# Optimization experiments

Hardware: AMD Instinct MI355X
Metric: run time of the kernel (lower is better)

Reference implementation:

```python
import jax, jax.numpy as jnp
import numpy as np

B, N, D, E = 2, 50000, 64, 800000


def setup_inputs() -> dict:
    key = jax.random.key(0)
    k = jax.random.split(key, 6)
    return {
        "prev_embeddings": jax.random.normal(k[0], (B, N, D), dtype=jnp.float32),
        "edges_ij": jax.random.randint(k[1], (E, 2), 0, N, dtype=jnp.int64 if jax.config.jax_enable_x64 else jnp.int32),
        "node_features_embeddings": jax.random.normal(k[2], (B, N, D), dtype=jnp.float32),
        "edge_features_embeddings": jax.random.normal(k[3], (B, N, D), dtype=jnp.float32),
        "edge_status": jax.random.uniform(k[4], (E,), dtype=jnp.float32),
        "W": jax.random.normal(k[5], (D, D), dtype=jnp.float32) / np.sqrt(D).astype(np.float32),
    }


def reference(prev_embeddings, edges_ij, node_features_embeddings, edge_features_embeddings, edge_status, W):
    # prev_embeddings: (B, N, D); edges_ij: (E, 2); edge_status: (E,) in [0,1]; W: (D, D) theta2 weight (no bias)
    u = edges_ij[:, 0]
    v = edges_ij[:, 1]
    g = edge_status.astype(prev_embeddings.dtype).reshape(1, -1, 1)  # broadcast (1,E,1) over batch
    h_u = prev_embeddings[:, u, :] * g  # gather source endpoint, gate
    h_v = prev_embeddings[:, v, :] * g  # gather dest endpoint, gate
    # scatter-add gated messages in both directions: nbr[b, v] += h_u, nbr[b, u] += h_v
    nbr = jnp.zeros_like(prev_embeddings).at[:, v, :].add(h_u).at[:, u, :].add(h_v)
    x2 = jnp.einsum('bnd,ed->bne', nbr, W)  # Linear(D,D,bias=False): nbr @ W.T
    return jax.nn.leaky_relu(node_features_embeddings + x2 + edge_features_embeddings)
```

## Files before the change

kernel.cpp:

```cpp
#include <hip/hip_runtime.h>

constexpr int B = 2;
constexpr int N = 50000;
constexpr int D = 64;
constexpr int E = 800000;
constexpr int CAP = 96;
constexpr int XG = 8;
constexpr int NPG = N / XG;
constexpr int ECHUNKS = E / 256;

constexpr int ROWS_PER_WAVE = 25;
constexpr int PGROUPS = 125;
constexpr int TOTAL_GROUPS = ECHUNKS + PGROUPS;

__device__ __forceinline__ unsigned f2bf(float f) {
    unsigned u = __float_as_uint(f);
    return (u + 0x7FFFu + ((u >> 16) & 1u)) >> 16;
}
__device__ __forceinline__ float bfhi2f(unsigned bits) {
    return __uint_as_float(bits & 0xFFFF0000u);
}
__device__ __forceinline__ float bflo2f(unsigned bits) {
    return __uint_as_float(bits << 16);
}

__global__ __launch_bounds__(256) void build_pgemm_fused(
    const int2* __restrict__ edges, const float* __restrict__ status,
    int* __restrict__ counts, unsigned* __restrict__ slots,
    const float* __restrict__ prev, const float* __restrict__ W,
    unsigned* __restrict__ P32)
{
    int grp = blockIdx.x >> 3;
    int sub8 = blockIdx.x & 7;
    int t = threadIdx.x;

    int nm = grp / 26;
    int pos = grp % 26;

    if (pos < 25) {
        int chunk = nm * 25 + pos;
        int e = chunk * 256 + t;
        int2 uv = edges[e];
        unsigned gb = f2bf(status[e]) << 16;
        if (uv.x / NPG == sub8) {
            int p = atomicAdd(&counts[uv.x], 1);
            if (p < CAP) slots[(size_t)uv.x * CAP + p] = gb | (unsigned)uv.y;
        }
        if (uv.y / NPG == sub8) {
            int p = atomicAdd(&counts[uv.y], 1);
            if (p < CAP) slots[(size_t)uv.y * CAP + p] = gb | (unsigned)uv.x;
        }
    } else {
        int pb = nm * 8 + sub8;
        int wave = t >> 6, lane = t & 63;

        const float4* W4 = (const float4*)W;
        float4 w[16];
#pragma unroll
        for (int q = 0; q < 16; ++q) w[q] = W4[lane * 16 + q];

        int row0 = pb * (4 * ROWS_PER_WAVE) + wave * ROWS_PER_WAVE;
        for (int r = 0; r < ROWS_PER_WAVE; ++r) {
            int row = __builtin_amdgcn_readfirstlane(row0 + r);
            const float* pr = prev + (size_t)row * D;

            float acc = 0.f;
#pragma unroll
            for (int d = 0; d < D; ++d) {
                const float4& wq = w[d >> 2];
                float wd = (d & 3) == 0 ? wq.x : (d & 3) == 1 ? wq.y
                         : (d & 3) == 2 ? wq.z : wq.w;
                acc += pr[d] * wd;
            }

            float partner = __shfl_xor(acc, 1, 64);
            if ((lane & 1) == 0) {
                P32[(size_t)row * 32 + (lane >> 1)] = f2bf(acc) | (f2bf(partner) << 16);
            }
        }
    }
}

__global__ __launch_bounds__(256) void gather_final(
    const uint4* __restrict__ P4,
    const int* __restrict__ counts,
    const unsigned* __restrict__ slots,
    const float* __restrict__ node,
    const float* __restrict__ edgef,
    float* __restrict__ out)
{
    __shared__ float xs[4][2][D];

    int t = threadIdx.x;
    int wave = t >> 6, lane = t & 63;
    int n = blockIdx.x * 4 + wave;
    int j = lane & 7;
    int sub = lane >> 3;

    int cnt = min(counts[n], CAP);
    size_t sbase = (size_t)n * CAP;

    float a0[8], a1[8];
#pragma unroll
    for (int i = 0; i < 8; ++i) { a0[i] = 0.f; a1[i] = 0.f; }

    for (int k = sub; k < cnt; k += 8) {
        unsigned ent = slots[sbase + k];
        float g = bfhi2f(ent);
        unsigned nb = ent & 0xFFFFu;
        uint4 r0 = P4[(size_t)nb * 8 + j];
        uint4 r1 = P4[((size_t)N + nb) * 8 + j];
        a0[0] += g * bflo2f(r0.x); a0[1] += g * bfhi2f(r0.x);
        a0[2] += g * bflo2f(r0.y); a0[3] += g * bfhi2f(r0.y);
        a0[4] += g * bflo2f(r0.z); a0[5] += g * bfhi2f(r0.z);
        a0[6] += g * bflo2f(r0.w); a0[7] += g * bfhi2f(r0.w);
        a1[0] += g * bflo2f(r1.x); a1[1] += g * bfhi2f(r1.x);
        a1[2] += g * bflo2f(r1.y); a1[3] += g * bfhi2f(r1.y);
        a1[4] += g * bflo2f(r1.z); a1[5] += g * bfhi2f(r1.z);
        a1[6] += g * bflo2f(r1.w); a1[7] += g * bfhi2f(r1.w);
    }

#pragma unroll
    for (int m = 8; m <= 32; m <<= 1) {
#pragma unroll
        for (int i = 0; i < 8; ++i) {
            a0[i] += __shfl_xor(a0[i], m, 64);
            a1[i] += __shfl_xor(a1[i], m, 64);
        }
    }

    if (sub == 0) {
        *(float4*)&xs[wave][0][j * 8]     = make_float4(a0[0], a0[1], a0[2], a0[3]);
        *(float4*)&xs[wave][0][j * 8 + 4] = make_float4(a0[4], a0[5], a0[6], a0[7]);
        *(float4*)&xs[wave][1][j * 8]     = make_float4(a1[0], a1[1], a1[2], a1[3]);
        *(float4*)&xs[wave][1][j * 8 + 4] = make_float4(a1[4], a1[5], a1[6], a1[7]);
    }
    float s0 = xs[wave][0][lane];
    float s1 = xs[wave][1][lane];

    size_t b0 = (size_t)n * D + lane;
    size_t b1 = (size_t)N * D + b0;
    float y0 = node[b0] + s0 + edgef[b0];
    float y1 = node[b1] + s1 + edgef[b1];
    out[b0] = (y0 >= 0.f) ? y0 : 0.01f * y0;
    out[b1] = (y1 >= 0.f) ? y1 : 0.01f * y1;
}

__device__ inline void atomic_add4(float* p, float4 val, float g) {
    atomicAdd(p + 0, val.x * g);
    atomicAdd(p + 1, val.y * g);
    atomicAdd(p + 2, val.z * g);
    atomicAdd(p + 3, val.w * g);
}

__global__ __launch_bounds__(256) void scatter_kernel(
    const float* __restrict__ prev,
    const int2* __restrict__ edges,
    const float* __restrict__ status,
    float* __restrict__ nbr)
{
    int idx = blockIdx.x * 256 + threadIdx.x;
    int e = idx >> 4;
    int q = idx & 15;
    if (e >= E) return;
    int2 uv = edges[e];
    float g = status[e];
    const float4* p0 = (const float4*)prev;
    const float4* p1 = (const float4*)(prev + (size_t)N * D);
    float4 pu0 = p0[(size_t)uv.x * 16 + q];
    float4 pv0 = p0[(size_t)uv.y * 16 + q];
    float4 pu1 = p1[(size_t)uv.x * 16 + q];
    float4 pv1 = p1[(size_t)uv.y * 16 + q];
    float* n0 = nbr;
    float* n1 = nbr + (size_t)N * D;
    int off_v = uv.y * D + q * 4;
    int off_u = uv.x * D + q * 4;
    atomic_add4(n0 + off_v, pu0, g);
    atomic_add4(n0 + off_u, pv0, g);
    atomic_add4(n1 + off_v, pu1, g);
    atomic_add4(n1 + off_u, pv1, g);
}

__global__ __launch_bounds__(256) void gemm_relu_kernel(
    float* __restrict__ out,
    const float* __restrict__ node,
    const float* __restrict__ edgef,
    const float* __restrict__ W)
{
    __shared__ float Wl[D][D + 1];
    __shared__ float xs[4][D];
    int t = threadIdx.x;
    for (int i = t; i < D * D; i += 256) Wl[i >> 6][i & 63] = W[i];
    int wave = t >> 6, lane = t & 63;
    int row = blockIdx.x * 4 + wave;
    size_t base = (size_t)row * D;
    float x = out[base + lane];
    xs[wave][lane] = x;
    __syncthreads();
    float acc = 0.f;
#pragma unroll
    for (int d = 0; d < D; ++d) acc += xs[wave][d] * Wl[lane][d];
    float y = node[base + lane] + acc + edgef[base + lane];
    out[base + lane] = (y >= 0.f) ? y : 0.01f * y;
}

extern "C" void kernel_launch(void* const* d_in, const int* in_sizes, int n_in,
                              void* d_out, int out_size, void* d_ws, size_t ws_size,
                              hipStream_t stream) {
    const float* prev   = (const float*)d_in[0];
    const int*   edges  = (const int*)d_in[1];
    const float* node   = (const float*)d_in[2];
    const float* edgef  = (const float*)d_in[3];
    const float* status = (const float*)d_in[4];
    const float* W      = (const float*)d_in[5];
    float* out = (float*)d_out;

    const int2* edges2 = (const int2*)edges;

    size_t slots_bytes  = (size_t)N * CAP * sizeof(unsigned);
    size_t counts_bytes = (size_t)N * sizeof(int);
    size_t p_bytes      = (size_t)B * N * 32 * sizeof(unsigned);
    size_t need = slots_bytes + counts_bytes + p_bytes;

    if (ws_size >= need) {
        unsigned* slots = (unsigned*)d_ws;
        int* counts = (int*)((char*)d_ws + slots_bytes);
        unsigned* P32 = (unsigned*)((char*)d_ws + slots_bytes + counts_bytes);

        hipMemsetAsync(counts, 0, counts_bytes, stream);
        build_pgemm_fused<<<TOTAL_GROUPS * 8, 256, 0, stream>>>(
            edges2, status, counts, slots, prev, W, P32);
        gather_final<<<N / 4, 256, 0, stream>>>(
            (const uint4*)P32, counts, slots, node, edgef, out);
    } else {
        hipMemsetAsync(out, 0, (size_t)B * N * D * sizeof(float), stream);
        scatter_kernel<<<(E * 16) / 256, 256, 0, stream>>>(prev, edges2, status, out);
        gemm_relu_kernel<<<(B * N) / 4, 256, 0, stream>>>(out, node, edgef, W);
    }
}
```

Measured before the change: 312.8 us.

## Pad per-node counters to 64B stride and process two edges per thread in build

Counter array entries are spaced 16 ints apart so each node's atomic counter occupies its own 64-byte line, which should reduce atomic contention and false sharing on shared cache lines. The memset grows to 3.2 MB, and a fallback to unpadded counters is kept for small workspaces. Each build thread now handles two edges with all atomics issued before the slot stores, to raise memory-level parallelism. The interleave of build and P-GEMM blocks changes from 25:1 to 12:1, plus a tail of build-only groups.

Result: faster. 272.7 us (-12.8%).

```diff
diff --git a/kernel.cpp b/kernel.cpp
--- a/kernel.cpp
+++ b/kernel.cpp
@@ -7,11 +7,12 @@
 constexpr int CAP = 96;
 constexpr int XG = 8;
 constexpr int NPG = N / XG;
-constexpr int ECHUNKS = E / 256;
+constexpr int CSTRIDE_PAD = 16;
 
 constexpr int ROWS_PER_WAVE = 25;
+constexpr int BGROUPS = 1563;
 constexpr int PGROUPS = 125;
-constexpr int TOTAL_GROUPS = ECHUNKS + PGROUPS;
+constexpr int TOTAL_GROUPS = BGROUPS + PGROUPS;
 
 __device__ __forceinline__ unsigned f2bf(float f) {
     unsigned u = __float_as_uint(f);
@@ -28,30 +29,44 @@
     const int2* __restrict__ edges, const float* __restrict__ status,
     int* __restrict__ counts, unsigned* __restrict__ slots,
     const float* __restrict__ prev, const float* __restrict__ W,
-    unsigned* __restrict__ P32)
+    unsigned* __restrict__ P32, int cstride)
 {
     int grp = blockIdx.x >> 3;
     int sub8 = blockIdx.x & 7;
     int t = threadIdx.x;
 
-    int nm = grp / 26;
-    int pos = grp % 26;
-
-    if (pos < 25) {
-        int chunk = nm * 25 + pos;
-        int e = chunk * 256 + t;
-        int2 uv = edges[e];
-        unsigned gb = f2bf(status[e]) << 16;
-        if (uv.x / NPG == sub8) {
-            int p = atomicAdd(&counts[uv.x], 1);
-            if (p < CAP) slots[(size_t)uv.x * CAP + p] = gb | (unsigned)uv.y;
-        }
-        if (uv.y / NPG == sub8) {
-            int p = atomicAdd(&counts[uv.y], 1);
-            if (p < CAP) slots[(size_t)uv.y * CAP + p] = gb | (unsigned)uv.x;
-        }
+    int cyc = grp / 13, pos = grp % 13;
+    bool is_pgemm = (pos == 12) && (grp < PGROUPS * 13);
+
+    if (!is_pgemm) {
+        int b = (grp < PGROUPS * 13) ? (cyc * 12 + pos) : (1500 + (grp - PGROUPS * 13));
+        int e0 = b * 512 + t;
+        int e1 = e0 + 256;
+        bool has1 = (e1 < E);
+
+        int2 uv0 = edges[e0];
+        float st0 = status[e0];
+        int2 uv1 = has1 ? edges[e1] : uv0;
+        float st1 = has1 ? status[e1] : 0.f;
+        unsigned gb0 = f2bf(st0) << 16;
+        unsigned gb1 = f2bf(st1) << 16;
+
+        bool du0 = (uv0.x / NPG == sub8);
+        bool dv0 = (uv0.y / NPG == sub8);
+        bool du1 = has1 && (uv1.x / NPG == sub8);
+        bool dv1 = has1 && (uv1.y / NPG == sub8);
+
+        int pu0 = CAP, pv0 = CAP, pu1 = CAP, pv1 = CAP;
+        if (du0) pu0 = atomicAdd(&counts[(size_t)uv0.x * cstride], 1);
+        if (dv0) pv0 = atomicAdd(&counts[(size_t)uv0.y * cstride], 1);
+        if (du1) pu1 = atomicAdd(&counts[(size_t)uv1.x * cstride], 1);
+        if (dv1) pv1 = atomicAdd(&counts[(size_t)uv1.y * cstride], 1);
+        if (du0 && pu0 < CAP) slots[(size_t)uv0.x * CAP + pu0] = gb0 | (unsigned)uv0.y;
+        if (dv0 && pv0 < CAP) slots[(size_t)uv0.y * CAP + pv0] = gb0 | (unsigned)uv0.x;
+        if (du1 && pu1 < CAP) slots[(size_t)uv1.x * CAP + pu1] = gb1 | (unsigned)uv1.y;
+        if (dv1 && pv1 < CAP) slots[(size_t)uv1.y * CAP + pv1] = gb1 | (unsigned)uv1.x;
     } else {
-        int pb = nm * 8 + sub8;
+        int pb = cyc * 8 + sub8;
         int wave = t >> 6, lane = t & 63;
 
         const float4* W4 = (const float4*)W;
@@ -87,7 +102,7 @@
     const unsigned* __restrict__ slots,
     const float* __restrict__ node,
     const float* __restrict__ edgef,
-    float* __restrict__ out)
+    float* __restrict__ out, int cstride)
 {
     __shared__ float xs[4][2][D];
 
@@ -97,7 +112,7 @@
     int j = lane & 7;
     int sub = lane >> 3;
 
-    int cnt = min(counts[n], CAP);
+    int cnt = min(counts[(size_t)n * cstride], CAP);
     size_t sbase = (size_t)n * CAP;
 
     float a0[8], a1[8];
@@ -218,23 +233,30 @@
     const int2* edges2 = (const int2*)edges;
 
     size_t slots_bytes  = (size_t)N * CAP * sizeof(unsigned);
-    size_t counts_bytes = (size_t)N * sizeof(int);
     size_t p_bytes      = (size_t)B * N * 32 * sizeof(unsigned);
-    size_t need = slots_bytes + counts_bytes + p_bytes;
-
-    if (ws_size >= need) {
-        unsigned* slots = (unsigned*)d_ws;
-        int* counts = (int*)((char*)d_ws + slots_bytes);
-        unsigned* P32 = (unsigned*)((char*)d_ws + slots_bytes + counts_bytes);
-
-        hipMemsetAsync(counts, 0, counts_bytes, stream);
-        build_pgemm_fused<<<TOTAL_GROUPS * 8, 256, 0, stream>>>(
-            edges2, status, counts, slots, prev, W, P32);
-        gather_final<<<N / 4, 256, 0, stream>>>(
-            (const uint4*)P32, counts, slots, node, edgef, out);
+    size_t counts_pad   = (size_t)N * CSTRIDE_PAD * sizeof(int);
+    size_t counts_min   = (size_t)N * sizeof(int);
+
+    int cstride;
+    size_t counts_bytes;
+    if (ws_size >= slots_bytes + counts_pad + p_bytes) {
+        cstride = CSTRIDE_PAD; counts_bytes = counts_pad;
+    } else if (ws_size >= slots_bytes + counts_min + p_bytes) {
+        cstride = 1; counts_bytes = counts_min;
     } else {
         hipMemsetAsync(out, 0, (size_t)B * N * D * sizeof(float), stream);
         scatter_kernel<<<(E * 16) / 256, 256, 0, stream>>>(prev, edges2, status, out);
         gemm_relu_kernel<<<(B * N) / 4, 256, 0, stream>>>(out, node, edgef, W);
-    }
-}
+        return;
+    }
+
+    unsigned* slots = (unsigned*)d_ws;
+    int* counts = (int*)((char*)d_ws + slots_bytes);
+    unsigned* P32 = (unsigned*)((char*)d_ws + slots_bytes + counts_bytes);
+
+    hipMemsetAsync(counts, 0, counts_bytes, stream);
+    build_pgemm_fused<<<TOTAL_GROUPS * 8, 256, 0, stream>>>(
+        edges2, status, counts, slots, prev, W, P32, cstride);
+    gather_final<<<N / 4, 256, 0, stream>>>(
+        (const uint4*)P32, counts, slots, node, edgef, out, cstride);
+}
```
